# Optimization experiments

Measured on AMD Instinct MI355X. Metric: run time of the kernel, lower is better.

The kernel has to match this reference:

```python
import jax, jax.numpy as jnp
import numpy as np

N_NODES = 100000
N_EDGES = 1600000
NFEAT = 128
NHID = 128
NCLASS = 40


def gcn_conv(x, W, b, src, dst, n_nodes):
    """PyG-style GCNConv: x' = D^{-1/2}(A+I)D^{-1/2} (x W) + b."""
    h = x @ W  # [N, out]
    loop = jnp.arange(n_nodes, dtype=src.dtype)
    s = jnp.concatenate([src, loop])  # add self-loops
    d = jnp.concatenate([dst, loop])
    deg = jax.ops.segment_sum(jnp.ones_like(s, dtype=h.dtype), d, num_segments=n_nodes)
    dinv = jnp.where(deg > 0, jax.lax.rsqrt(deg), 0.0)
    norm = dinv[s] * dinv[d]  # [E+N]
    msg = h[s] * norm[:, None]  # gather + scale
    out = jax.ops.segment_sum(msg, d, num_segments=n_nodes)  # scatter-add
    return out + b


def setup_inputs() -> dict:
    key = jax.random.key(0)
    ks = jax.random.split(key, 6)
    x = jax.random.normal(ks[0], (N_NODES, NFEAT), dtype=jnp.float32)
    edge_index = jax.random.randint(ks[1], (2, N_EDGES), 0, N_NODES, dtype=jnp.int64)
    sc1 = 1.0 / np.sqrt(NFEAT)
    sc2 = 1.0 / np.sqrt(NHID)
    W1 = jax.random.normal(ks[2], (NFEAT, NHID), dtype=jnp.float32) * sc1
    b1 = jnp.zeros((NHID,), dtype=jnp.float32)
    Wm = jax.random.normal(ks[3], (NHID, NHID), dtype=jnp.float32) * sc2
    bm = jnp.zeros((NHID,), dtype=jnp.float32)
    W2 = jax.random.normal(ks[4], (NHID, NCLASS), dtype=jnp.float32) * sc2
    b2 = jnp.zeros((NCLASS,), dtype=jnp.float32)
    return {"x": x, "edge_index": edge_index, "W1": W1, "b1": b1,
            "Wm": Wm, "bm": bm, "W2": W2, "b2": b2}


def reference(x, edge_index, W1, b1, Wm, bm, W2, b2):
    # StandGCNX forward, eval mode (dropout = identity)
    src, dst = edge_index[0], edge_index[1]
    n = x.shape[0]
    h = jax.nn.relu(gcn_conv(x, W1, b1, src, dst, n))
    h = jax.nn.relu(gcn_conv(h, Wm, bm, src, dst, n))
    out = gcn_conv(h, W2, b2, src, dst, n)
    return out
```

## Files before the change

### kernel.cpp

```cpp
#include <hip/hip_runtime.h>
#include <hip/hip_bf16.h>

typedef __attribute__((ext_vector_type(8))) short bf16x8;
typedef __attribute__((ext_vector_type(4))) float f32x4;

__device__ __forceinline__ ushort bf16rne(float f) {
    uint u = __float_as_uint(f);
    return (ushort)((u + 0x7fffu + ((u >> 16) & 1u)) >> 16);
}
__device__ __forceinline__ void unpack2(uint p, float& a, float& b) {
    a = __uint_as_float(p << 16);
    b = __uint_as_float(p & 0xffff0000u);
}


__global__ __launch_bounds__(256) void k_bhist(const int* __restrict__ dst,
                                               int* __restrict__ bcnt, int E) {
    __shared__ int hist[512];
    int t = threadIdx.x;
    hist[t] = 0; hist[t + 256] = 0;
    __syncthreads();
    int off = blockIdx.x * 4096;
    int cnt = min(4096, E - off);
    for (int i = t; i < cnt; i += 256) atomicAdd(&hist[dst[off + i] >> 8], 1);
    __syncthreads();
    if (hist[t]) atomicAdd(&bcnt[t], hist[t]);
    if (hist[t + 256]) atomicAdd(&bcnt[t + 256], hist[t + 256]);
}

__global__ void k_bscan(const int* __restrict__ bcnt, int* __restrict__ bbase,
                        int* __restrict__ bcur, int nbuck) {
    __shared__ int s[512];
    int t = threadIdx.x;
    s[t] = (t < nbuck) ? bcnt[t] : 0;
    __syncthreads();
    for (int d = 1; d < 512; d <<= 1) {
        int u = (t >= d) ? s[t - d] : 0;
        __syncthreads();
        if (t >= d) s[t] += u;
        __syncthreads();
    }
    int excl = (t == 0) ? 0 : s[t - 1];
    bbase[t] = excl;
    if (t < nbuck) bcur[t] = excl;
    if (t == 511) bbase[512] = s[511];
}

__global__ __launch_bounds__(256) void k_binpack(const int* __restrict__ src,
                                                 const int* __restrict__ dst,
                                                 int* __restrict__ bcur,
                                                 uint* __restrict__ pairbuf,
                                                 int E, int nbuck) {
    __shared__ int hist[512];
    __shared__ int scn[512];
    __shared__ int cur[512];
    __shared__ int gbase[512];
    __shared__ uint sorted[4096];
    int t = threadIdx.x;
    int off = blockIdx.x * 4096;
    int cnt = min(4096, E - off);

    hist[t] = 0; hist[t + 256] = 0;
    __syncthreads();
    for (int i = t; i < cnt; i += 256) {
        int b = dst[off + i] >> 8;
        atomicAdd(&hist[b], 1);
    }
    __syncthreads();
    scn[t] = hist[t]; scn[t + 256] = hist[t + 256];
    __syncthreads();
    for (int d = 1; d < 256; d <<= 1) {
        int u0 = (t >= d) ? scn[t - d] : 0;
        int u1 = (t >= d) ? scn[256 + t - d] : 0;
        __syncthreads();
        if (t >= d) { scn[t] += u0; scn[256 + t] += u1; }
        __syncthreads();
    }
    int tot0 = scn[255];
    scn[256 + t] += tot0;
    __syncthreads();
    cur[t] = (t == 0) ? 0 : scn[t - 1];
    cur[t + 256] = scn[t + 255];
    if (t < nbuck && hist[t] > 0) gbase[t] = atomicAdd(&bcur[t], hist[t]);
    int t2 = t + 256;
    if (t2 < nbuck && hist[t2] > 0) gbase[t2] = atomicAdd(&bcur[t2], hist[t2]);
    __syncthreads();
    for (int i = t; i < cnt; i += 256) {
        int d = dst[off + i];
        int s = src[off + i];
        int b = d >> 8;
        int pos = atomicAdd(&cur[b], 1);
        sorted[pos] = ((uint)(d & 255) << 24) | (uint)s;
    }
    __syncthreads();
    int wid = t >> 6, lane = t & 63;
    for (int b = wid; b < nbuck; b += 4) {
        int n = hist[b];
        if (n == 0) continue;
        int ls = (b == 0) ? 0 : scn[b - 1];
        int gb = gbase[b];
        for (int j = lane; j < n; j += 64)
            pairbuf[gb + j] = sorted[ls + j];
    }
}

#define CSR_CAP 5632
__global__ __launch_bounds__(256) void k_csrbuild(const uint* __restrict__ pairbuf,
                                                  const int* __restrict__ bbase,
                                                  int* __restrict__ rowptr,
                                                  float* __restrict__ dinv,
                                                  int* __restrict__ csr,
                                                  int N, int nbuck) {
    __shared__ int lhist[256];
    __shared__ int scn[256];
    __shared__ int lcur[256];
    __shared__ int lcsr[CSR_CAP];
    int b = blockIdx.x;
    int base = b << 8;
    int nn = min(256, N - base);
    int lo = bbase[b], hi = bbase[b + 1];
    int cnt = hi - lo;
    int t = threadIdx.x;
    lhist[t] = 0;
    __syncthreads();
    for (int i = t; i < cnt; i += 256) atomicAdd(&lhist[pairbuf[lo + i] >> 24], 1);
    __syncthreads();
    int mydeg = lhist[t];
    scn[t] = mydeg;
    __syncthreads();
    for (int d = 1; d < 256; d <<= 1) {
        int u = (t >= d) ? scn[t - d] : 0;
        __syncthreads();
        if (t >= d) scn[t] += u;
        __syncthreads();
    }
    int excl = (t == 0) ? 0 : scn[t - 1];
    lcur[t] = excl;
    if (t < nn) {
        rowptr[base + t] = lo + excl;
        dinv[base + t] = rsqrtf((float)(mydeg + 1));
    }
    if (b == nbuck - 1 && t == 0) rowptr[N] = hi;
    __syncthreads();
    if (cnt <= CSR_CAP) {
        for (int i = t; i < cnt; i += 256) {
            uint p = pairbuf[lo + i];
            int pos = atomicAdd(&lcur[p >> 24], 1);
            lcsr[pos] = (int)(p & 0xFFFFFFu);
        }
        __syncthreads();
        for (int i = t; i < cnt; i += 256) csr[lo + i] = lcsr[i];
    } else {
        for (int i = t; i < cnt; i += 256) {
            uint p = pairbuf[lo + i];
            int pos = lo + atomicAdd(&lcur[p >> 24], 1);
            csr[pos] = (int)(p & 0xFFFFFFu);
        }
    }
}


__global__ void k_castT_all(const float* __restrict__ W1, const float* __restrict__ Wm,
                            const float* __restrict__ W2, ushort* __restrict__ w1t,
                            ushort* __restrict__ wmt, ushort* __restrict__ w2t) {
    int b = blockIdx.x;
    int t = threadIdx.x;
    if (b < 64) {
        int i = b * 256 + t; int k = i >> 7, n = i & 127;
        w1t[n * 128 + k] = bf16rne(W1[k * 128 + n]);
    } else if (b < 128) {
        int i = (b - 64) * 256 + t; int k = i >> 7, n = i & 127;
        wmt[n * 128 + k] = bf16rne(Wm[k * 128 + n]);
    } else {
        int i = (b - 128) * 256 + t;
        if (i < 6144) {
            int n = i >> 7, k = i & 127;
            w2t[n * 128 + k] = (n < 40) ? bf16rne(W2[k * 40 + n]) : (ushort)0;
        }
    }
}


__global__ __launch_bounds__(256) void k_gemm1(const float* __restrict__ A,
                                               const ushort* __restrict__ Wt,
                                               const float* __restrict__ dinv,
                                               ushort* __restrict__ C, int M) {
    int t = threadIdx.x;
    int wave = t >> 6, lane = t & 63;
    int m16 = lane & 15, quad = lane >> 4;
    int rowA = blockIdx.x * 64 + wave * 16 + m16;
    int rA = min(rowA, M - 1);
    const float4* A4 = (const float4*)A;

    f32x4 acc[8];
#pragma unroll
    for (int i = 0; i < 8; i++) acc[i] = (f32x4){0.f, 0.f, 0.f, 0.f};

#pragma unroll
    for (int it = 0; it < 4; it++) {
        float4 f0 = A4[(size_t)rA * 32 + 8 * it + 2 * quad];
        float4 f1 = A4[(size_t)rA * 32 + 8 * it + 2 * quad + 1];
        bf16x8 af;
        af[0] = (short)bf16rne(f0.x); af[1] = (short)bf16rne(f0.y);
        af[2] = (short)bf16rne(f0.z); af[3] = (short)bf16rne(f0.w);
        af[4] = (short)bf16rne(f1.x); af[5] = (short)bf16rne(f1.y);
        af[6] = (short)bf16rne(f1.z); af[7] = (short)bf16rne(f1.w);
#pragma unroll
        for (int nt = 0; nt < 8; nt++) {
            bf16x8 bfr = *(const bf16x8*)(Wt + (size_t)(nt * 16 + m16) * 128 + it * 32 + quad * 8);
            acc[nt] = __builtin_amdgcn_mfma_f32_16x16x32_bf16(af, bfr, acc[nt], 0, 0, 0);
        }
    }
    int rowBase = blockIdx.x * 64 + wave * 16 + quad * 4;
    float dnv[4];
#pragma unroll
    for (int r = 0; r < 4; r++) dnv[r] = dinv[min(rowBase + r, M - 1)];
#pragma unroll
    for (int nt = 0; nt < 8; nt++) {
        int col = nt * 16 + m16;
#pragma unroll
        for (int r = 0; r < 4; r++) {
            int row = rowBase + r;
            if (row < M) C[(size_t)row * 128 + col] = bf16rne(acc[nt][r] * dnv[r]);
        }
    }
}


template <int NT>
__device__ __forceinline__ void fused_agg_gemm(const ushort* __restrict__ g,
                                               const float* __restrict__ dinv,
                                               const int* __restrict__ rowptr,
                                               const int* __restrict__ csr,
                                               const float* __restrict__ bias,
                                               const ushort* __restrict__ Wt,
                                               ushort* __restrict__ C,
                                               int M, int ccols) {
    __shared__ ushort hs[32][136];
    __shared__ int nextNode;
    int t = threadIdx.x;
    if (t == 0) nextNode = 0;
    int l = t & 15;
    const uint4* g16 = (const uint4*)g;
    float4 bb0 = ((const float4*)bias)[2 * l];
    float4 bb1 = ((const float4*)bias)[2 * l + 1];
    __syncthreads();

    for (;;) {
        int idx = 0;
        if (l == 0) idx = atomicAdd(&nextNode, 1);
        idx = __shfl(idx, (t & 63) & ~15, 64);
        if (idx >= 32) break;
        int node = blockIdx.x * 32 + idx;
        int nd = min(node, M - 1);
        float dn = dinv[nd];
        float a[8];
        {
            uint4 p = g16[(size_t)nd * 16 + l];
            unpack2(p.x, a[0], a[1]); unpack2(p.y, a[2], a[3]);
            unpack2(p.z, a[4], a[5]); unpack2(p.w, a[6], a[7]);
        }
        int e0 = rowptr[nd], e1 = rowptr[nd + 1];
        int e = e0;
        for (; e + 4 <= e1; e += 4) {
            int s0 = csr[e], s1 = csr[e + 1], s2 = csr[e + 2], s3 = csr[e + 3];
            uint4 p0 = g16[(size_t)s0 * 16 + l];
            uint4 p1 = g16[(size_t)s1 * 16 + l];
            uint4 p2 = g16[(size_t)s2 * 16 + l];
            uint4 p3 = g16[(size_t)s3 * 16 + l];
            float u, v;
            unpack2(p0.x, u, v); a[0] += u; a[1] += v;
            unpack2(p0.y, u, v); a[2] += u; a[3] += v;
            unpack2(p0.z, u, v); a[4] += u; a[5] += v;
            unpack2(p0.w, u, v); a[6] += u; a[7] += v;
            unpack2(p1.x, u, v); a[0] += u; a[1] += v;
            unpack2(p1.y, u, v); a[2] += u; a[3] += v;
            unpack2(p1.z, u, v); a[4] += u; a[5] += v;
            unpack2(p1.w, u, v); a[6] += u; a[7] += v;
            unpack2(p2.x, u, v); a[0] += u; a[1] += v;
            unpack2(p2.y, u, v); a[2] += u; a[3] += v;
            unpack2(p2.z, u, v); a[4] += u; a[5] += v;
            unpack2(p2.w, u, v); a[6] += u; a[7] += v;
            unpack2(p3.x, u, v); a[0] += u; a[1] += v;
            unpack2(p3.y, u, v); a[2] += u; a[3] += v;
            unpack2(p3.z, u, v); a[4] += u; a[5] += v;
            unpack2(p3.w, u, v); a[6] += u; a[7] += v;
        }
        for (; e < e1; e++) {
            int s = csr[e];
            uint4 p = g16[(size_t)s * 16 + l];
            float u, v;
            unpack2(p.x, u, v); a[0] += u; a[1] += v;
            unpack2(p.y, u, v); a[2] += u; a[3] += v;
            unpack2(p.z, u, v); a[4] += u; a[5] += v;
            unpack2(p.w, u, v); a[6] += u; a[7] += v;
        }
        float o0 = fmaxf(a[0] * dn + bb0.x, 0.f);
        float o1 = fmaxf(a[1] * dn + bb0.y, 0.f);
        float o2 = fmaxf(a[2] * dn + bb0.z, 0.f);
        float o3 = fmaxf(a[3] * dn + bb0.w, 0.f);
        float o4 = fmaxf(a[4] * dn + bb1.x, 0.f);
        float o5 = fmaxf(a[5] * dn + bb1.y, 0.f);
        float o6 = fmaxf(a[6] * dn + bb1.z, 0.f);
        float o7 = fmaxf(a[7] * dn + bb1.w, 0.f);
        uint4 qv;
        qv.x = (uint)bf16rne(o0) | ((uint)bf16rne(o1) << 16);
        qv.y = (uint)bf16rne(o2) | ((uint)bf16rne(o3) << 16);
        qv.z = (uint)bf16rne(o4) | ((uint)bf16rne(o5) << 16);
        qv.w = (uint)bf16rne(o6) | ((uint)bf16rne(o7) << 16);
        *(uint4*)&hs[idx][l * 8] = qv;
    }
    __syncthreads();

    int wave = t >> 6, lane = t & 63;
    int m16 = lane & 15, quad = lane >> 4;
    int rowHalf = wave & 1;
    int ntHalf = wave >> 1;
    constexpr int NTH = (NT + 1) / 2;
    int ntStart = ntHalf * NTH;
    int ntEnd = ntHalf ? NT : NTH;

    f32x4 acc[NTH];
#pragma unroll
    for (int i = 0; i < NTH; i++) acc[i] = (f32x4){0.f, 0.f, 0.f, 0.f};
#pragma unroll
    for (int it = 0; it < 4; it++) {
        bf16x8 af = *(const bf16x8*)&hs[rowHalf * 16 + m16][it * 32 + quad * 8];
        for (int nt = ntStart; nt < ntEnd; nt++) {
            bf16x8 bfr = *(const bf16x8*)(Wt + (size_t)(nt * 16 + m16) * 128 + it * 32 + quad * 8);
            acc[nt - ntStart] = __builtin_amdgcn_mfma_f32_16x16x32_bf16(af, bfr, acc[nt - ntStart], 0, 0, 0);
        }
    }
    int rowBase = blockIdx.x * 32 + rowHalf * 16 + quad * 4;
    float dnv[4];
#pragma unroll
    for (int r = 0; r < 4; r++) dnv[r] = dinv[min(rowBase + r, M - 1)];
    for (int nt = ntStart; nt < ntEnd; nt++) {
        int col = nt * 16 + m16;
        if (col >= ccols) continue;
#pragma unroll
        for (int r = 0; r < 4; r++) {
            int row = rowBase + r;
            if (row < M) C[(size_t)row * ccols + col] = bf16rne(acc[nt - ntStart][r] * dnv[r]);
        }
    }
}

__global__ __launch_bounds__(256) void k_fusedA(const ushort* __restrict__ g,
                                                const float* __restrict__ dinv,
                                                const int* __restrict__ rowptr,
                                                const int* __restrict__ csr,
                                                const float* __restrict__ bias,
                                                const ushort* __restrict__ Wt,
                                                ushort* __restrict__ C, int M) {
    fused_agg_gemm<8>(g, dinv, rowptr, csr, bias, Wt, C, M, 128);
}

__global__ __launch_bounds__(256) void k_fusedB(const ushort* __restrict__ g,
                                                const float* __restrict__ dinv,
                                                const int* __restrict__ rowptr,
                                                const int* __restrict__ csr,
                                                const float* __restrict__ bias,
                                                const ushort* __restrict__ Wt,
                                                ushort* __restrict__ C, int M) {
    fused_agg_gemm<3>(g, dinv, rowptr, csr, bias, Wt, C, M, 40);
}


__global__ __launch_bounds__(256) void k_agg40_b(const ushort* __restrict__ g3,
                                                 const float* __restrict__ dinv,
                                                 const int* __restrict__ rowptr,
                                                 const int* __restrict__ csr,
                                                 const float* __restrict__ bias,
                                                 float* __restrict__ out, int N) {
    int t = threadIdx.x;
    if (t >= 250) return;
    int grp = t / 10;
    int l = t - grp * 10;
    int node = blockIdx.x * 25 + grp;
    if (node >= N) return;
    const uint2* gp = (const uint2*)g3;
    float dn = dinv[node];
    float a0, a1, a2, a3;
    {
        uint2 p = gp[(size_t)node * 10 + l];
        unpack2(p.x, a0, a1);
        unpack2(p.y, a2, a3);
    }
    int e0 = rowptr[node], e1 = rowptr[node + 1];
    int e = e0;
    for (; e + 4 <= e1; e += 4) {
        int s0 = csr[e], s1 = csr[e + 1], s2 = csr[e + 2], s3 = csr[e + 3];
        uint2 p0 = gp[(size_t)s0 * 10 + l];
        uint2 p1 = gp[(size_t)s1 * 10 + l];
        uint2 p2 = gp[(size_t)s2 * 10 + l];
        uint2 p3 = gp[(size_t)s3 * 10 + l];
        float u, v;
        unpack2(p0.x, u, v); a0 += u; a1 += v;
        unpack2(p0.y, u, v); a2 += u; a3 += v;
        unpack2(p1.x, u, v); a0 += u; a1 += v;
        unpack2(p1.y, u, v); a2 += u; a3 += v;
        unpack2(p2.x, u, v); a0 += u; a1 += v;
        unpack2(p2.y, u, v); a2 += u; a3 += v;
        unpack2(p3.x, u, v); a0 += u; a1 += v;
        unpack2(p3.y, u, v); a2 += u; a3 += v;
    }
    for (; e < e1; e++) {
        int s = csr[e];
        uint2 p = gp[(size_t)s * 10 + l];
        float u, v;
        unpack2(p.x, u, v); a0 += u; a1 += v;
        unpack2(p.y, u, v); a2 += u; a3 += v;
    }
    float4 bb = ((const float4*)bias)[l];
    float4 o;
    o.x = a0 * dn + bb.x;
    o.y = a1 * dn + bb.y;
    o.z = a2 * dn + bb.z;
    o.w = a3 * dn + bb.w;
    ((float4*)out)[(size_t)node * 10 + l] = o;
}


extern "C" void kernel_launch(void* const* d_in, const int* in_sizes, int n_in,
                              void* d_out, int out_size, void* d_ws, size_t ws_size,
                              hipStream_t stream) {
    const float* x  = (const float*)d_in[0];
    const int* eidx = (const int*)d_in[1];
    const float* W1 = (const float*)d_in[2];
    const float* b1 = (const float*)d_in[3];
    const float* Wm = (const float*)d_in[4];
    const float* bm = (const float*)d_in[5];
    const float* W2 = (const float*)d_in[6];
    const float* b2 = (const float*)d_in[7];
    float* out = (float*)d_out;

    int N = in_sizes[0] / 128;
    int E = in_sizes[1] / 2;
    const int* src = eidx;
    const int* dst = eidx + E;
    int nbuck = (N + 255) >> 8;

    char* ws = (char*)d_ws;
    size_t off = 0;
    auto alloc = [&](size_t bytes) -> void* {
        void* p = ws + off;
        off += (bytes + 255) & ~(size_t)255;
        return p;
    };
    float*  dinv    = (float*)alloc((size_t)N * 4);
    int*    rowptr  = (int*)alloc(((size_t)N + 1) * 4);
    int*    csr     = (int*)alloc((size_t)E * 4);
    uint*   pairbuf = (uint*)alloc((size_t)E * 4);
    int*    bcnt    = (int*)alloc(512 * 4);
    int*    bbase   = (int*)alloc(513 * 4);
    int*    bcur    = (int*)alloc(512 * 4);
    ushort* w1t     = (ushort*)alloc(128 * 128 * 2);
    ushort* wmt     = (ushort*)alloc(128 * 128 * 2);
    ushort* w2t     = (ushort*)alloc(48 * 128 * 2);
    ushort* gbuf    = (ushort*)alloc((size_t)N * 128 * 2);
    ushort* gbuf2   = (ushort*)alloc((size_t)N * 128 * 2);
    ushort* g3      = (ushort*)alloc((size_t)N * 40 * 2);

    hipMemsetAsync(bcnt, 0, 512 * 4, stream);
    k_bhist<<<(E + 4095) / 4096, 256, 0, stream>>>(dst, bcnt, E);
    k_bscan<<<1, 512, 0, stream>>>(bcnt, bbase, bcur, nbuck);
    k_binpack<<<(E + 4095) / 4096, 256, 0, stream>>>(src, dst, bcur, pairbuf, E, nbuck);
    k_csrbuild<<<nbuck, 256, 0, stream>>>(pairbuf, bbase, rowptr, dinv, csr, N, nbuck);
    k_castT_all<<<152, 256, 0, stream>>>(W1, Wm, W2, w1t, wmt, w2t);

    int gblk64 = (N + 63) / 64;
    int gblk32 = (N + 31) / 32;
    k_gemm1<<<gblk64, 256, 0, stream>>>(x, w1t, dinv, gbuf, N);
    k_fusedA<<<gblk32, 256, 0, stream>>>(gbuf, dinv, rowptr, csr, b1, wmt, gbuf2, N);
    k_fusedB<<<gblk32, 256, 0, stream>>>(gbuf2, dinv, rowptr, csr, bm, w2t, g3, N);
    k_agg40_b<<<(N + 24) / 25, 256, 0, stream>>>(g3, dinv, rowptr, csr, b2, out, N);
}
```

Before: 382.5 us.

## Merge weight cast into histogram kernel and GEMM1 into CSR build

```diff
diff --git a/kernel.cpp b/kernel.cpp
--- a/kernel.cpp
+++ b/kernel.cpp
@@ -14,13 +14,36 @@
 }
 
 
-__global__ __launch_bounds__(256) void k_bhist(const int* __restrict__ dst,
-                                               int* __restrict__ bcnt, int E) {
+__global__ __launch_bounds__(256) void k_pre1(const float* __restrict__ W1,
+                                              const float* __restrict__ Wm,
+                                              const float* __restrict__ W2,
+                                              ushort* __restrict__ w1t,
+                                              ushort* __restrict__ wmt,
+                                              ushort* __restrict__ w2t,
+                                              const int* __restrict__ dst,
+                                              int* __restrict__ bcnt, int E) {
     __shared__ int hist[512];
-    int t = threadIdx.x;
+    int b = blockIdx.x;
+    int t = threadIdx.x;
+    if (b < 152) {
+        if (b < 64) {
+            int i = b * 256 + t; int k = i >> 7, n = i & 127;
+            w1t[n * 128 + k] = bf16rne(W1[k * 128 + n]);
+        } else if (b < 128) {
+            int i = (b - 64) * 256 + t; int k = i >> 7, n = i & 127;
+            wmt[n * 128 + k] = bf16rne(Wm[k * 128 + n]);
+        } else {
+            int i = (b - 128) * 256 + t;
+            if (i < 6144) {
+                int n = i >> 7, k = i & 127;
+                w2t[n * 128 + k] = (n < 40) ? bf16rne(W2[k * 40 + n]) : (ushort)0;
+            }
+        }
+        return;
+    }
     hist[t] = 0; hist[t + 256] = 0;
     __syncthreads();
-    int off = blockIdx.x * 4096;
+    int off = (b - 152) * 4096;
     int cnt = min(4096, E - off);
     for (int i = t; i < cnt; i += 256) atomicAdd(&hist[dst[off + i] >> 8], 1);
     __syncthreads();
@@ -104,23 +127,65 @@
     }
 }
 
+
 #define CSR_CAP 5632
-__global__ __launch_bounds__(256) void k_csrbuild(const uint* __restrict__ pairbuf,
-                                                  const int* __restrict__ bbase,
-                                                  int* __restrict__ rowptr,
-                                                  float* __restrict__ dinv,
-                                                  int* __restrict__ csr,
-                                                  int N, int nbuck) {
+__global__ __launch_bounds__(256) void k_mega(const uint* __restrict__ pairbuf,
+                                              const int* __restrict__ bbase,
+                                              int* __restrict__ rowptr,
+                                              float* __restrict__ dinv,
+                                              int* __restrict__ csr,
+                                              int N, int nbuck,
+                                              const float* __restrict__ A,
+                                              const ushort* __restrict__ Wt,
+                                              ushort* __restrict__ C, int M) {
     __shared__ int lhist[256];
     __shared__ int scn[256];
     __shared__ int lcur[256];
     __shared__ int lcsr[CSR_CAP];
+    int t = threadIdx.x;
+    if ((int)blockIdx.x >= nbuck) {
+        int blk = blockIdx.x - nbuck;
+        int wave = t >> 6, lane = t & 63;
+        int m16 = lane & 15, quad = lane >> 4;
+        int rowA = blk * 64 + wave * 16 + m16;
+        int rA = min(rowA, M - 1);
+        const float4* A4 = (const float4*)A;
+
+        f32x4 acc[8];
+#pragma unroll
+        for (int i = 0; i < 8; i++) acc[i] = (f32x4){0.f, 0.f, 0.f, 0.f};
+#pragma unroll
+        for (int it = 0; it < 4; it++) {
+            float4 f0 = A4[(size_t)rA * 32 + 8 * it + 2 * quad];
+            float4 f1 = A4[(size_t)rA * 32 + 8 * it + 2 * quad + 1];
+            bf16x8 af;
+            af[0] = (short)bf16rne(f0.x); af[1] = (short)bf16rne(f0.y);
+            af[2] = (short)bf16rne(f0.z); af[3] = (short)bf16rne(f0.w);
+            af[4] = (short)bf16rne(f1.x); af[5] = (short)bf16rne(f1.y);
+            af[6] = (short)bf16rne(f1.z); af[7] = (short)bf16rne(f1.w);
+#pragma unroll
+            for (int nt = 0; nt < 8; nt++) {
+                bf16x8 bfr = *(const bf16x8*)(Wt + (size_t)(nt * 16 + m16) * 128 + it * 32 + quad * 8);
+                acc[nt] = __builtin_amdgcn_mfma_f32_16x16x32_bf16(af, bfr, acc[nt], 0, 0, 0);
+            }
+        }
+        int rowBase = blk * 64 + wave * 16 + quad * 4;
+#pragma unroll
+        for (int nt = 0; nt < 8; nt++) {
+            int col = nt * 16 + m16;
+#pragma unroll
+            for (int r = 0; r < 4; r++) {
+                int row = rowBase + r;
+                if (row < M) C[(size_t)row * 128 + col] = bf16rne(acc[nt][r]);
+            }
+        }
+        return;
+    }
     int b = blockIdx.x;
     int base = b << 8;
     int nn = min(256, N - base);
     int lo = bbase[b], hi = bbase[b + 1];
     int cnt = hi - lo;
-    int t = threadIdx.x;
     lhist[t] = 0;
     __syncthreads();
     for (int i = t; i < cnt; i += 256) atomicAdd(&lhist[pairbuf[lo + i] >> 24], 1);
@@ -155,73 +220,6 @@
             uint p = pairbuf[lo + i];
             int pos = lo + atomicAdd(&lcur[p >> 24], 1);
             csr[pos] = (int)(p & 0xFFFFFFu);
-        }
-    }
-}
-
-
-__global__ void k_castT_all(const float* __restrict__ W1, const float* __restrict__ Wm,
-                            const float* __restrict__ W2, ushort* __restrict__ w1t,
-                            ushort* __restrict__ wmt, ushort* __restrict__ w2t) {
-    int b = blockIdx.x;
-    int t = threadIdx.x;
-    if (b < 64) {
-        int i = b * 256 + t; int k = i >> 7, n = i & 127;
-        w1t[n * 128 + k] = bf16rne(W1[k * 128 + n]);
-    } else if (b < 128) {
-        int i = (b - 64) * 256 + t; int k = i >> 7, n = i & 127;
-        wmt[n * 128 + k] = bf16rne(Wm[k * 128 + n]);
-    } else {
-        int i = (b - 128) * 256 + t;
-        if (i < 6144) {
-            int n = i >> 7, k = i & 127;
-            w2t[n * 128 + k] = (n < 40) ? bf16rne(W2[k * 40 + n]) : (ushort)0;
-        }
-    }
-}
-
-
-__global__ __launch_bounds__(256) void k_gemm1(const float* __restrict__ A,
-                                               const ushort* __restrict__ Wt,
-                                               const float* __restrict__ dinv,
-                                               ushort* __restrict__ C, int M) {
-    int t = threadIdx.x;
-    int wave = t >> 6, lane = t & 63;
-    int m16 = lane & 15, quad = lane >> 4;
-    int rowA = blockIdx.x * 64 + wave * 16 + m16;
-    int rA = min(rowA, M - 1);
-    const float4* A4 = (const float4*)A;
-
-    f32x4 acc[8];
-#pragma unroll
-    for (int i = 0; i < 8; i++) acc[i] = (f32x4){0.f, 0.f, 0.f, 0.f};
-
-#pragma unroll
-    for (int it = 0; it < 4; it++) {
-        float4 f0 = A4[(size_t)rA * 32 + 8 * it + 2 * quad];
-        float4 f1 = A4[(size_t)rA * 32 + 8 * it + 2 * quad + 1];
-        bf16x8 af;
-        af[0] = (short)bf16rne(f0.x); af[1] = (short)bf16rne(f0.y);
-        af[2] = (short)bf16rne(f0.z); af[3] = (short)bf16rne(f0.w);
-        af[4] = (short)bf16rne(f1.x); af[5] = (short)bf16rne(f1.y);
-        af[6] = (short)bf16rne(f1.z); af[7] = (short)bf16rne(f1.w);
-#pragma unroll
-        for (int nt = 0; nt < 8; nt++) {
-            bf16x8 bfr = *(const bf16x8*)(Wt + (size_t)(nt * 16 + m16) * 128 + it * 32 + quad * 8);
-            acc[nt] = __builtin_amdgcn_mfma_f32_16x16x32_bf16(af, bfr, acc[nt], 0, 0, 0);
-        }
-    }
-    int rowBase = blockIdx.x * 64 + wave * 16 + quad * 4;
-    float dnv[4];
-#pragma unroll
-    for (int r = 0; r < 4; r++) dnv[r] = dinv[min(rowBase + r, M - 1)];
-#pragma unroll
-    for (int nt = 0; nt < 8; nt++) {
-        int col = nt * 16 + m16;
-#pragma unroll
-        for (int r = 0; r < 4; r++) {
-            int row = rowBase + r;
-            if (row < M) C[(size_t)row * 128 + col] = bf16rne(acc[nt][r] * dnv[r]);
         }
     }
 }
@@ -257,43 +255,48 @@
         float a[8];
         {
             uint4 p = g16[(size_t)nd * 16 + l];
-            unpack2(p.x, a[0], a[1]); unpack2(p.y, a[2], a[3]);
-            unpack2(p.z, a[4], a[5]); unpack2(p.w, a[6], a[7]);
+            float u, v;
+            unpack2(p.x, u, v); a[0] = u * dn; a[1] = v * dn;
+            unpack2(p.y, u, v); a[2] = u * dn; a[3] = v * dn;
+            unpack2(p.z, u, v); a[4] = u * dn; a[5] = v * dn;
+            unpack2(p.w, u, v); a[6] = u * dn; a[7] = v * dn;
         }
         int e0 = rowptr[nd], e1 = rowptr[nd + 1];
         int e = e0;
         for (; e + 4 <= e1; e += 4) {
             int s0 = csr[e], s1 = csr[e + 1], s2 = csr[e + 2], s3 = csr[e + 3];
+            float w0 = dinv[s0], w1 = dinv[s1], w2 = dinv[s2], w3 = dinv[s3];
             uint4 p0 = g16[(size_t)s0 * 16 + l];
             uint4 p1 = g16[(size_t)s1 * 16 + l];
             uint4 p2 = g16[(size_t)s2 * 16 + l];
             uint4 p3 = g16[(size_t)s3 * 16 + l];
             float u, v;
-            unpack2(p0.x, u, v); a[0] += u; a[1] += v;
-            unpack2(p0.y, u, v); a[2] += u; a[3] += v;
-            unpack2(p0.z, u, v); a[4] += u; a[5] += v;
-            unpack2(p0.w, u, v); a[6] += u; a[7] += v;
-            unpack2(p1.x, u, v); a[0] += u; a[1] += v;
-            unpack2(p1.y, u, v); a[2] += u; a[3] += v;
-            unpack2(p1.z, u, v); a[4] += u; a[5] += v;
-            unpack2(p1.w, u, v); a[6] += u; a[7] += v;
-            unpack2(p2.x, u, v); a[0] += u; a[1] += v;
-            unpack2(p2.y, u, v); a[2] += u; a[3] += v;
-            unpack2(p2.z, u, v); a[4] += u; a[5] += v;
-            unpack2(p2.w, u, v); a[6] += u; a[7] += v;
-            unpack2(p3.x, u, v); a[0] += u; a[1] += v;
-            unpack2(p3.y, u, v); a[2] += u; a[3] += v;
-            unpack2(p3.z, u, v); a[4] += u; a[5] += v;
-            unpack2(p3.w, u, v); a[6] += u; a[7] += v;
+            unpack2(p0.x, u, v); a[0] += u * w0; a[1] += v * w0;
+            unpack2(p0.y, u, v); a[2] += u * w0; a[3] += v * w0;
+            unpack2(p0.z, u, v); a[4] += u * w0; a[5] += v * w0;
+            unpack2(p0.w, u, v); a[6] += u * w0; a[7] += v * w0;
+            unpack2(p1.x, u, v); a[0] += u * w1; a[1] += v * w1;
+            unpack2(p1.y, u, v); a[2] += u * w1; a[3] += v * w1;
+            unpack2(p1.z, u, v); a[4] += u * w1; a[5] += v * w1;
+            unpack2(p1.w, u, v); a[6] += u * w1; a[7] += v * w1;
+            unpack2(p2.x, u, v); a[0] += u * w2; a[1] += v * w2;
+            unpack2(p2.y, u, v); a[2] += u * w2; a[3] += v * w2;
+            unpack2(p2.z, u, v); a[4] += u * w2; a[5] += v * w2;
+            unpack2(p2.w, u, v); a[6] += u * w2; a[7] += v * w2;
+            unpack2(p3.x, u, v); a[0] += u * w3; a[1] += v * w3;
+            unpack2(p3.y, u, v); a[2] += u * w3; a[3] += v * w3;
+            unpack2(p3.z, u, v); a[4] += u * w3; a[5] += v * w3;
+            unpack2(p3.w, u, v); a[6] += u * w3; a[7] += v * w3;
         }
         for (; e < e1; e++) {
             int s = csr[e];
+            float w = dinv[s];
             uint4 p = g16[(size_t)s * 16 + l];
             float u, v;
-            unpack2(p.x, u, v); a[0] += u; a[1] += v;
-            unpack2(p.y, u, v); a[2] += u; a[3] += v;
-            unpack2(p.z, u, v); a[4] += u; a[5] += v;
-            unpack2(p.w, u, v); a[6] += u; a[7] += v;
+            unpack2(p.x, u, v); a[0] += u * w; a[1] += v * w;
+            unpack2(p.y, u, v); a[2] += u * w; a[3] += v * w;
+            unpack2(p.z, u, v); a[4] += u * w; a[5] += v * w;
+            unpack2(p.w, u, v); a[6] += u * w; a[7] += v * w;
         }
         float o0 = fmaxf(a[0] * dn + bb0.x, 0.f);
         float o1 = fmaxf(a[1] * dn + bb0.y, 0.f);
@@ -332,16 +335,13 @@
         }
     }
     int rowBase = blockIdx.x * 32 + rowHalf * 16 + quad * 4;
-    float dnv[4];
-#pragma unroll
-    for (int r = 0; r < 4; r++) dnv[r] = dinv[min(rowBase + r, M - 1)];
     for (int nt = ntStart; nt < ntEnd; nt++) {
         int col = nt * 16 + m16;
         if (col >= ccols) continue;
 #pragma unroll
         for (int r = 0; r < 4; r++) {
             int row = rowBase + r;
-            if (row < M) C[(size_t)row * ccols + col] = bf16rne(acc[nt - ntStart][r] * dnv[r]);
+            if (row < M) C[(size_t)row * ccols + col] = bf16rne(acc[nt - ntStart][r]);
         }
     }
 }
@@ -384,33 +384,36 @@
     float a0, a1, a2, a3;
     {
         uint2 p = gp[(size_t)node * 10 + l];
-        unpack2(p.x, a0, a1);
-        unpack2(p.y, a2, a3);
+        float u, v;
+        unpack2(p.x, u, v); a0 = u * dn; a1 = v * dn;
+        unpack2(p.y, u, v); a2 = u * dn; a3 = v * dn;
     }
     int e0 = rowptr[node], e1 = rowptr[node + 1];
     int e = e0;
     for (; e + 4 <= e1; e += 4) {
         int s0 = csr[e], s1 = csr[e + 1], s2 = csr[e + 2], s3 = csr[e + 3];
+        float w0 = dinv[s0], w1 = dinv[s1], w2 = dinv[s2], w3 = dinv[s3];
         uint2 p0 = gp[(size_t)s0 * 10 + l];
         uint2 p1 = gp[(size_t)s1 * 10 + l];
         uint2 p2 = gp[(size_t)s2 * 10 + l];
         uint2 p3 = gp[(size_t)s3 * 10 + l];
         float u, v;
-        unpack2(p0.x, u, v); a0 += u; a1 += v;
-        unpack2(p0.y, u, v); a2 += u; a3 += v;
-        unpack2(p1.x, u, v); a0 += u; a1 += v;
-        unpack2(p1.y, u, v); a2 += u; a3 += v;
-        unpack2(p2.x, u, v); a0 += u; a1 += v;
-        unpack2(p2.y, u, v); a2 += u; a3 += v;
-        unpack2(p3.x, u, v); a0 += u; a1 += v;
-        unpack2(p3.y, u, v); a2 += u; a3 += v;
+        unpack2(p0.x, u, v); a0 += u * w0; a1 += v * w0;
+        unpack2(p0.y, u, v); a2 += u * w0; a3 += v * w0;
+        unpack2(p1.x, u, v); a0 += u * w1; a1 += v * w1;
+        unpack2(p1.y, u, v); a2 += u * w1; a3 += v * w1;
+        unpack2(p2.x, u, v); a0 += u * w2; a1 += v * w2;
+        unpack2(p2.y, u, v); a2 += u * w2; a3 += v * w2;
+        unpack2(p3.x, u, v); a0 += u * w3; a1 += v * w3;
+        unpack2(p3.y, u, v); a2 += u * w3; a3 += v * w3;
     }
     for (; e < e1; e++) {
         int s = csr[e];
+        float w = dinv[s];
         uint2 p = gp[(size_t)s * 10 + l];
         float u, v;
-        unpack2(p.x, u, v); a0 += u; a1 += v;
-        unpack2(p.y, u, v); a2 += u; a3 += v;
+        unpack2(p.x, u, v); a0 += u * w; a1 += v * w;
+        unpack2(p.y, u, v); a2 += u * w; a3 += v * w;
     }
     float4 bb = ((const float4*)bias)[l];
     float4 o;
@@ -440,6 +443,7 @@
     const int* src = eidx;
     const int* dst = eidx + E;
     int nbuck = (N + 255) >> 8;
+    int ntile = (E + 4095) / 4096;
 
     char* ws = (char*)d_ws;
     size_t off = 0;
@@ -462,16 +466,15 @@
     ushort* gbuf2   = (ushort*)alloc((size_t)N * 128 * 2);
     ushort* g3      = (ushort*)alloc((size_t)N * 40 * 2);
 
-    hipMemsetAsync(bcnt, 0, 512 * 4, stream);
-    k_bhist<<<(E + 4095) / 4096, 256, 0, stream>>>(dst, bcnt, E);
-    k_bscan<<<1, 512, 0, stream>>>(bcnt, bbase, bcur, nbuck);
-    k_binpack<<<(E + 4095) / 4096, 256, 0, stream>>>(src, dst, bcur, pairbuf, E, nbuck);
-    k_csrbuild<<<nbuck, 256, 0, stream>>>(pairbuf, bbase, rowptr, dinv, csr, N, nbuck);
-    k_castT_all<<<152, 256, 0, stream>>>(W1, Wm, W2, w1t, wmt, w2t);
-
     int gblk64 = (N + 63) / 64;
     int gblk32 = (N + 31) / 32;
-    k_gemm1<<<gblk64, 256, 0, stream>>>(x, w1t, dinv, gbuf, N);
+
+    hipMemsetAsync(bcnt, 0, 512 * 4, stream);
+    k_pre1<<<152 + ntile, 256, 0, stream>>>(W1, Wm, W2, w1t, wmt, w2t, dst, bcnt, E);
+    k_bscan<<<1, 512, 0, stream>>>(bcnt, bbase, bcur, nbuck);
+    k_binpack<<<ntile, 256, 0, stream>>>(src, dst, bcur, pairbuf, E, nbuck);
+    k_mega<<<nbuck + gblk64, 256, 0, stream>>>(pairbuf, bbase, rowptr, dinv, csr,
+                                               N, nbuck, x, w1t, gbuf, N);
     k_fusedA<<<gblk32, 256, 0, stream>>>(gbuf, dinv, rowptr, csr, b1, wmt, gbuf2, N);
     k_fusedB<<<gblk32, 256, 0, stream>>>(gbuf2, dinv, rowptr, csr, bm, w2t, g3, N);
     k_agg40_b<<<(N + 24) / 25, 256, 0, stream>>>(g3, dinv, rowptr, csr, b2, out, N);
```

Result: slower. 391.0 us (+2.2%).
